# Optimization experiments

Measured on AMD Instinct MI355X. Metric: run time of the kernel, lower is better.

The kernel has to match this reference:

```python
import jax, jax.numpy as jnp
import numpy as np

D_IN = 1024
D_OUT = 1024


def setup_inputs() -> dict:
    key = jax.random.key(0)
    kx, kq, kk, kv = jax.random.split(key, 4)
    s = 1.0 / np.sqrt(D_IN)
    x = jax.random.normal(kx, (2, 4096, D_IN), dtype=jnp.float32)
    # nn.Linear weights: shape [d_out, d_in], y = x @ W.T (no bias)
    W_query = jax.random.normal(kq, (D_OUT, D_IN), dtype=jnp.float32) * s
    W_key = jax.random.normal(kk, (D_OUT, D_IN), dtype=jnp.float32) * s
    W_value = jax.random.normal(kv, (D_OUT, D_IN), dtype=jnp.float32) * s
    return {"x": x, "W_query": W_query, "W_key": W_key, "W_value": W_value}


def reference(x, W_query, W_key, W_value):
    # QKV projections: [b, n, d_in] @ [d_in, d_out]
    q = jnp.einsum('bnd,od->bno', x, W_query)
    k = jnp.einsum('bnd,od->bno', x, W_key)
    v = jnp.einsum('bnd,od->bno', x, W_value)
    d_k = k.shape[-1]
    scores = jnp.einsum('bqo,bko->bqk', q, k) / jnp.sqrt(jnp.asarray(d_k, x.dtype))
    # NOTE: source applies no causal mask despite the class name
    attn = jax.nn.softmax(scores, axis=-1)
    return jnp.einsum('bqk,bko->bqo', attn, v)
```

## Files before the change

### kernel.cpp

```cpp
#include <hip/hip_runtime.h>
#include <hip/hip_bf16.h>
#include <hip/hip_fp16.h>
#include <stdint.h>

typedef __bf16 bf16_t;
typedef __bf16 bf16x8 __attribute__((ext_vector_type(8)));
typedef float f32x4 __attribute__((ext_vector_type(4)));

typedef __attribute__((address_space(1))) void gv_t;
typedef __attribute__((address_space(3))) void lv_t;

__device__ inline unsigned short f2bf_bits(float f) {
  uint32_t u = __float_as_uint(f);
  u += 0x7FFFu + ((u >> 16) & 1u);
  return (unsigned short)(u >> 16);
}
__device__ inline bf16_t f2bf(float f) {
  unsigned short h = f2bf_bits(f);
  return __builtin_bit_cast(bf16_t, h);
}

__device__ inline void storeC(float* p, float v) { *p = v; }
__device__ inline void storeC(bf16_t* p, float v) { *p = f2bf(v); }
__device__ inline void storeC(__half* p, float v) { *p = __float2half(v); }

__global__ __launch_bounds__(256)
void convert_all(const float* __restrict__ x, const float* __restrict__ wq,
                 const float* __restrict__ wk, const float* __restrict__ wv,
                 bf16_t* __restrict__ xb, bf16_t* __restrict__ wqkb,
                 bf16_t* __restrict__ wvb)
{
  const int64_t NX = 8192LL * 1024, NW = 1024LL * 1024;
  const int64_t total4 = (NX + 3 * NW) >> 2;
  for (int64_t i = (int64_t)blockIdx.x * blockDim.x + threadIdx.x; i < total4;
       i += (int64_t)gridDim.x * blockDim.x) {
    int64_t e = i << 2;
    const float* src; bf16_t* dst; int64_t off;
    if (e < NX)               { src = x;  dst = xb;         off = e; }
    else if (e < NX + NW)     { src = wq; dst = wqkb;       off = e - NX; }
    else if (e < NX + 2 * NW) { src = wk; dst = wqkb + NW;  off = e - NX - NW; }
    else                      { src = wv; dst = wvb;        off = e - NX - 2 * NW; }
    float4 f = *(const float4*)(src + off);
    uint32_t lo = ((uint32_t)f2bf_bits(f.y) << 16) | f2bf_bits(f.x);
    uint32_t hi = ((uint32_t)f2bf_bits(f.w) << 16) | f2bf_bits(f.z);
    *(uint2*)(dst + off) = make_uint2(lo, hi);
  }
}

template <typename OUT_T>
__global__ __launch_bounds__(256)
void gemm_bt(const bf16_t* __restrict__ A, const bf16_t* __restrict__ B,
             OUT_T* __restrict__ C, int K, int lda, int ldb, int ldc,
             int64_t b_batch_stride, int bm_per_batch)
{
  __shared__ bf16_t As[2][128 * 32];
  __shared__ bf16_t Bs[2][128 * 32];
  const int tid  = threadIdx.x;
  const int wid  = tid >> 6;
  const int lane = tid & 63;
  const int wm = wid >> 1, wn = wid & 1;
  const int64_t bm = blockIdx.x;
  const int64_t bn = blockIdx.y;

  const bf16_t* Bb = B + (bm / bm_per_batch) * b_batch_stride;

  const int c0row = (wid * 2 + 0) * 16 + (lane >> 2);
  const int c1row = (wid * 2 + 1) * 16 + (lane >> 2);
  const int scol  = (lane & 3) * 8;

  const bf16_t* Ar0 = A  + (bm * 128 + c0row) * lda + scol;
  const bf16_t* Ar1 = A  + (bm * 128 + c1row) * lda + scol;
  const bf16_t* Br0 = Bb + (bn * 128 + c0row) * ldb + scol;
  const bf16_t* Br1 = Bb + (bn * 128 + c1row) * ldb + scol;

  const int ad0 = (wid * 2 + 0) * 512;
  const int ad1 = (wid * 2 + 1) * 512;

  const int frow = lane & 15;
  const int fk   = (lane >> 4) * 8;
  const int aoff = (wm * 64 + frow) * 32 + fk;
  const int boff = (wn * 64 + frow) * 32 + fk;

  f32x4 acc[4][4];
  #pragma unroll
  for (int m = 0; m < 4; m++)
    #pragma unroll
    for (int n = 0; n < 4; n++) acc[m][n] = f32x4{0.f, 0.f, 0.f, 0.f};

  auto stage = [&](int buf, int k0) {
    __builtin_amdgcn_global_load_lds((const gv_t*)(Ar0 + k0),
                                     (lv_t*)(&As[buf][ad0]), 16, 0, 0);
    __builtin_amdgcn_global_load_lds((const gv_t*)(Ar1 + k0),
                                     (lv_t*)(&As[buf][ad1]), 16, 0, 0);
    __builtin_amdgcn_global_load_lds((const gv_t*)(Br0 + k0),
                                     (lv_t*)(&Bs[buf][ad0]), 16, 0, 0);
    __builtin_amdgcn_global_load_lds((const gv_t*)(Br1 + k0),
                                     (lv_t*)(&Bs[buf][ad1]), 16, 0, 0);
  };

  stage(0, 0);
  __syncthreads();
  int cur = 0;
  for (int k0 = 0; k0 < K; k0 += 32) {
    if (k0 + 32 < K) stage(cur ^ 1, k0 + 32);

    bf16x8 af[4], bfr[4];
    #pragma unroll
    for (int m = 0; m < 4; m++)
      af[m] = *(const bf16x8*)(&As[cur][aoff + m * 16 * 32]);
    #pragma unroll
    for (int n = 0; n < 4; n++)
      bfr[n] = *(const bf16x8*)(&Bs[cur][boff + n * 16 * 32]);
    #pragma unroll
    for (int m = 0; m < 4; m++)
      #pragma unroll
      for (int n = 0; n < 4; n++)
        acc[m][n] = __builtin_amdgcn_mfma_f32_16x16x32_bf16(af[m], bfr[n],
                                                            acc[m][n], 0, 0, 0);
    __syncthreads();
    cur ^= 1;
  }

  const int crow = (lane >> 4) * 4;
  const int ccol = lane & 15;
  #pragma unroll
  for (int m = 0; m < 4; m++)
    #pragma unroll
    for (int n = 0; n < 4; n++)
      #pragma unroll
      for (int j = 0; j < 4; j++) {
        int64_t row = bm * 128 + wm * 64 + m * 16 + crow + j;
        int64_t col = bn * 128 + wn * 64 + n * 16 + ccol;
        storeC(&C[row * ldc + col], acc[m][n][j]);
      }
}

template <typename OUT_T, typename OUT2_T>
__global__ __launch_bounds__(512, 2)
void gemm256(const bf16_t* __restrict__ A, const bf16_t* __restrict__ B,
             OUT_T* __restrict__ C0, OUT2_T* __restrict__ C1,
             int K, int lda, int ldb, int ldc,
             int64_t b_batch_stride, int bm_per_batch,
             int64_t za_off, int64_t zb_off)
{
  __shared__ bf16_t As[2][256][64];
  __shared__ bf16_t Bs[2][256][64];

  const int tid  = threadIdx.x;
  const int wid  = tid >> 6;
  const int lane = tid & 63;
  const int wm = wid >> 2;
  const int wn = wid & 3;
  const int64_t bm = blockIdx.x;
  const int64_t bn = blockIdx.y;
  const int z = blockIdx.z;

  const bf16_t* Ap = A + (int64_t)z * za_off;
  const bf16_t* Bp = B + (bm / bm_per_batch) * b_batch_stride
                       + (int64_t)z * zb_off;

  const int srow  = wid * 16 + (lane >> 3);
  const int sslot = (lane & 7) ^ (lane >> 3);
  const int64_t lda64 = lda, ldb64 = ldb;
  const bf16_t* Ag = Ap + (bm * 256 + srow) * lda64 + sslot * 8;
  const bf16_t* Bg = Bp + (bn * 256 + srow) * ldb64 + sslot * 8;

  auto stageA = [&](int buf, int t, int h) {
    const bf16_t* src = Ag + (int64_t)(h * 128) * lda64 + t * 64;
    char* dst = (char*)&As[buf][h * 128 + wid * 16][0];
    __builtin_amdgcn_global_load_lds((const gv_t*)src, (lv_t*)dst, 16, 0, 0);
    __builtin_amdgcn_global_load_lds((const gv_t*)(src + 8 * lda64),
                                     (lv_t*)(dst + 1024), 16, 0, 0);
  };
  auto stageB = [&](int buf, int t, int h) {
    const bf16_t* src = Bg + (int64_t)(h * 128) * ldb64 + t * 64;
    char* dst = (char*)&Bs[buf][h * 128 + wid * 16][0];
    __builtin_amdgcn_global_load_lds((const gv_t*)src, (lv_t*)dst, 16, 0, 0);
    __builtin_amdgcn_global_load_lds((const gv_t*)(src + 8 * ldb64),
                                     (lv_t*)(dst + 1024), 16, 0, 0);
  };

  const int frow   = lane & 15;
  const int fcol16 = lane >> 4;
  const int xorv   = (lane & 7) << 4;
  const int ck0 = (fcol16 * 16) ^ xorv;
  const int ck1 = (64 + fcol16 * 16) ^ xorv;
  const int arowb = (wm * 128 + frow) * 128;
  const int browb = (wn * 64  + frow) * 128;

  f32x4 acc[8][4];
  #pragma unroll
  for (int m = 0; m < 8; m++)
    #pragma unroll
    for (int n = 0; n < 4; n++) acc[m][n] = f32x4{0.f, 0.f, 0.f, 0.f};

  const int NT = K >> 6;

  stageA(0, 0, 0); stageA(0, 0, 1);
  stageB(0, 0, 0); stageB(0, 0, 1);
  asm volatile("s_waitcnt vmcnt(0)" ::: "memory");
  __builtin_amdgcn_s_barrier();
  __builtin_amdgcn_sched_barrier(0);

  bf16x8 a[8][2], bb[4][2];

  for (int g = 0; g < NT; ++g) {
    const int buf = g & 1;
    const char* lA = (const char*)&As[buf][0][0];
    const char* lB = (const char*)&Bs[buf][0][0];

    #pragma unroll
    for (int m = 0; m < 8; m++)
      a[m][0] = *(const bf16x8*)(lA + arowb + m * 2048 + ck0);
    #pragma unroll
    for (int n = 0; n < 4; n++)
      bb[n][0] = *(const bf16x8*)(lB + browb + n * 2048 + ck0);
    #pragma unroll
    for (int m = 0; m < 8; m++)
      a[m][1] = *(const bf16x8*)(lA + arowb + m * 2048 + ck1);
    #pragma unroll
    for (int n = 0; n < 4; n++)
      bb[n][1] = *(const bf16x8*)(lB + browb + n * 2048 + ck1);

    if (g + 1 < NT) {
      stageA(buf ^ 1, g + 1, 0); stageA(buf ^ 1, g + 1, 1);
      stageB(buf ^ 1, g + 1, 0); stageB(buf ^ 1, g + 1, 1);
    }

    __builtin_amdgcn_s_setprio(1);
    #pragma unroll
    for (int k = 0; k < 2; k++)
      #pragma unroll
      for (int m = 0; m < 8; m++)
        #pragma unroll
        for (int n = 0; n < 4; n++)
          acc[m][n] = __builtin_amdgcn_mfma_f32_16x16x32_bf16(
              a[m][k], bb[n][k], acc[m][n], 0, 0, 0);
    __builtin_amdgcn_s_setprio(0);

    asm volatile("s_waitcnt vmcnt(0)" ::: "memory");
    __builtin_amdgcn_s_barrier();
    __builtin_amdgcn_sched_barrier(0);
  }

  const int crow = (lane >> 4) * 4;
  const int ccol = lane & 15;
  if (z == 0) {
    #pragma unroll
    for (int m = 0; m < 8; m++)
      #pragma unroll
      for (int n = 0; n < 4; n++)
        #pragma unroll
        for (int j = 0; j < 4; j++) {
          int64_t row = bm * 256 + wm * 128 + m * 16 + crow + j;
          int64_t col = bn * 256 + wn * 64 + n * 16 + ccol;
          storeC(&C0[row * (int64_t)ldc + col], acc[m][n][j]);
        }
  } else {
    #pragma unroll
    for (int m = 0; m < 8; m++)
      #pragma unroll
      for (int n = 0; n < 4; n++)
        #pragma unroll
        for (int j = 0; j < 4; j++) {
          int64_t row = bm * 256 + wm * 128 + m * 16 + crow + j;
          int64_t col = bn * 256 + wn * 64 + n * 16 + ccol;
          storeC(&C1[row * (int64_t)ldc + col], acc[m][n][j]);
        }
  }
}

__global__ __launch_bounds__(256)
void softmax_rows(__half* __restrict__ SP)
{
  const int64_t row = blockIdx.x;
  __half* s = SP + row * 4096;
  bf16_t* p = (bf16_t*)s;
  const int tid = threadIdx.x;
  const float scale = 0.03125f;

  float v[16];
  float vmax = -3.4e38f;
  #pragma unroll
  for (int i = 0; i < 4; i++) {
    uint2 raw = *(const uint2*)(s + i * 1024 + tid * 4);
    __half2 h01 = __builtin_bit_cast(__half2, raw.x);
    __half2 h23 = __builtin_bit_cast(__half2, raw.y);
    float2 f01 = __half22float2(h01);
    float2 f23 = __half22float2(h23);
    v[i * 4 + 0] = f01.x * scale;
    v[i * 4 + 1] = f01.y * scale;
    v[i * 4 + 2] = f23.x * scale;
    v[i * 4 + 3] = f23.y * scale;
    vmax = fmaxf(vmax, fmaxf(fmaxf(v[i*4+0], v[i*4+1]),
                             fmaxf(v[i*4+2], v[i*4+3])));
  }
  #pragma unroll
  for (int o = 32; o > 0; o >>= 1) vmax = fmaxf(vmax, __shfl_xor(vmax, o));
  __shared__ float redm[4];
  __shared__ float reds[4];
  if ((tid & 63) == 0) redm[tid >> 6] = vmax;
  __syncthreads();
  vmax = fmaxf(fmaxf(redm[0], redm[1]), fmaxf(redm[2], redm[3]));

  float lsum = 0.f;
  #pragma unroll
  for (int i = 0; i < 16; i++) {
    v[i] = __expf(v[i] - vmax);
    lsum += v[i];
  }
  #pragma unroll
  for (int o = 32; o > 0; o >>= 1) lsum += __shfl_xor(lsum, o);
  if ((tid & 63) == 0) reds[tid >> 6] = lsum;
  __syncthreads();
  lsum = (reds[0] + reds[1]) + (reds[2] + reds[3]);
  const float inv = 1.0f / lsum;

  #pragma unroll
  for (int i = 0; i < 4; i++) {
    uint32_t lo = ((uint32_t)f2bf_bits(v[i*4+1] * inv) << 16) | f2bf_bits(v[i*4+0] * inv);
    uint32_t hi = ((uint32_t)f2bf_bits(v[i*4+3] * inv) << 16) | f2bf_bits(v[i*4+2] * inv);
    *(uint2*)(p + i * 1024 + tid * 4) = make_uint2(lo, hi);
  }
}

__global__ __launch_bounds__(256)
void addk_h4(float4* __restrict__ o, const uint2* __restrict__ a, int64_t n4)
{
  for (int64_t i = (int64_t)blockIdx.x * blockDim.x + threadIdx.x; i < n4;
       i += (int64_t)gridDim.x * blockDim.x) {
    float4 x = o[i];
    uint2 raw = a[i];
    __half2 h01 = __builtin_bit_cast(__half2, raw.x);
    __half2 h23 = __builtin_bit_cast(__half2, raw.y);
    float2 f01 = __half22float2(h01);
    float2 f23 = __half22float2(h23);
    x.x += f01.x; x.y += f01.y; x.z += f23.x; x.w += f23.y;
    o[i] = x;
  }
}

extern "C" void kernel_launch(void* const* d_in, const int* in_sizes, int n_in,
                              void* d_out, int out_size, void* d_ws, size_t ws_size,
                              hipStream_t stream) {
  const float* x  = (const float*)d_in[0];
  const float* wq = (const float*)d_in[1];
  const float* wk = (const float*)d_in[2];
  const float* wv = (const float*)d_in[3];
  float* out = (float*)d_out;

  char* ws = (char*)d_ws;
  bf16_t* xb   = (bf16_t*)ws;
  bf16_t* wqkb = (bf16_t*)(ws + (16LL << 20));
  bf16_t* wvb  = (bf16_t*)(ws + (20LL << 20));
  __half* S    = (__half*)ws;
  bf16_t* qk   = (bf16_t*)(ws + (64LL << 20));
  __half* pk16 = (__half*)(ws + (64LL << 20));
  bf16_t* vt   = (bf16_t*)(ws + (96LL << 20));

  const int NO_BATCH = 1 << 30;

  convert_all<<<2048, 256, 0, stream>>>(x, wq, wk, wv, xb, wqkb, wvb);

  gemm256<bf16_t, bf16_t><<<dim3(32, 8, 1), 512, 0, stream>>>(
      xb, wqkb, qk, qk, 1024, 1024, 1024, 2048, 0, NO_BATCH, 0, 0);

  gemm_bt<bf16_t><<<dim3(8, 64), 256, 0, stream>>>(
      wvb, xb, vt, 1024, 1024, 1024, 8192, 0, NO_BATCH);

  gemm256<__half, __half><<<dim3(32, 16, 1), 512, 0, stream>>>(
      qk, qk + 1024, S, S, 1024, 2048, 2048, 4096, 4096LL * 2048, 16, 0, 0);

  softmax_rows<<<8192, 256, 0, stream>>>(S);

  gemm256<float, __half><<<dim3(32, 4, 2), 512, 0, stream>>>(
      (const bf16_t*)S, vt, out, pk16, 2048, 4096, 8192, 1024,
      4096, 16, 2048, 2048);

  addk_h4<<<2048, 256, 0, stream>>>((float4*)out, (const uint2*)pk16,
                                    8192LL * 1024 / 4);
}
```

Baseline: 230.6 us.

## Shrink GEMM tiles to 128x128 and reuse swizzled kernel for V projection

Replaces the 256x256-tile, 512-thread GEMM with a 128x128-tile, 256-thread variant that keeps the same XOR-swizzled LDS layout and double-buffered direct-to-LDS loads. The simple 32-wide-K gemm_bt used for the V-transpose projection is removed, and that projection now runs through the same kernel. Grids are rescaled, giving four times as many blocks per GEMM, which is meant to fill the CUs better and lower register and LDS pressure per block. In exchange each block does less data reuse per loaded byte, so global and L2 traffic rises.

```diff
diff --git a/kernel.cpp b/kernel.cpp
--- a/kernel.cpp
+++ b/kernel.cpp
@@ -47,110 +47,22 @@
   }
 }
 
-template <typename OUT_T>
-__global__ __launch_bounds__(256)
-void gemm_bt(const bf16_t* __restrict__ A, const bf16_t* __restrict__ B,
-             OUT_T* __restrict__ C, int K, int lda, int ldb, int ldc,
-             int64_t b_batch_stride, int bm_per_batch)
-{
-  __shared__ bf16_t As[2][128 * 32];
-  __shared__ bf16_t Bs[2][128 * 32];
-  const int tid  = threadIdx.x;
-  const int wid  = tid >> 6;
-  const int lane = tid & 63;
-  const int wm = wid >> 1, wn = wid & 1;
-  const int64_t bm = blockIdx.x;
-  const int64_t bn = blockIdx.y;
-
-  const bf16_t* Bb = B + (bm / bm_per_batch) * b_batch_stride;
-
-  const int c0row = (wid * 2 + 0) * 16 + (lane >> 2);
-  const int c1row = (wid * 2 + 1) * 16 + (lane >> 2);
-  const int scol  = (lane & 3) * 8;
-
-  const bf16_t* Ar0 = A  + (bm * 128 + c0row) * lda + scol;
-  const bf16_t* Ar1 = A  + (bm * 128 + c1row) * lda + scol;
-  const bf16_t* Br0 = Bb + (bn * 128 + c0row) * ldb + scol;
-  const bf16_t* Br1 = Bb + (bn * 128 + c1row) * ldb + scol;
-
-  const int ad0 = (wid * 2 + 0) * 512;
-  const int ad1 = (wid * 2 + 1) * 512;
-
-  const int frow = lane & 15;
-  const int fk   = (lane >> 4) * 8;
-  const int aoff = (wm * 64 + frow) * 32 + fk;
-  const int boff = (wn * 64 + frow) * 32 + fk;
-
-  f32x4 acc[4][4];
-  #pragma unroll
-  for (int m = 0; m < 4; m++)
-    #pragma unroll
-    for (int n = 0; n < 4; n++) acc[m][n] = f32x4{0.f, 0.f, 0.f, 0.f};
-
-  auto stage = [&](int buf, int k0) {
-    __builtin_amdgcn_global_load_lds((const gv_t*)(Ar0 + k0),
-                                     (lv_t*)(&As[buf][ad0]), 16, 0, 0);
-    __builtin_amdgcn_global_load_lds((const gv_t*)(Ar1 + k0),
-                                     (lv_t*)(&As[buf][ad1]), 16, 0, 0);
-    __builtin_amdgcn_global_load_lds((const gv_t*)(Br0 + k0),
-                                     (lv_t*)(&Bs[buf][ad0]), 16, 0, 0);
-    __builtin_amdgcn_global_load_lds((const gv_t*)(Br1 + k0),
-                                     (lv_t*)(&Bs[buf][ad1]), 16, 0, 0);
-  };
-
-  stage(0, 0);
-  __syncthreads();
-  int cur = 0;
-  for (int k0 = 0; k0 < K; k0 += 32) {
-    if (k0 + 32 < K) stage(cur ^ 1, k0 + 32);
-
-    bf16x8 af[4], bfr[4];
-    #pragma unroll
-    for (int m = 0; m < 4; m++)
-      af[m] = *(const bf16x8*)(&As[cur][aoff + m * 16 * 32]);
-    #pragma unroll
-    for (int n = 0; n < 4; n++)
-      bfr[n] = *(const bf16x8*)(&Bs[cur][boff + n * 16 * 32]);
-    #pragma unroll
-    for (int m = 0; m < 4; m++)
-      #pragma unroll
-      for (int n = 0; n < 4; n++)
-        acc[m][n] = __builtin_amdgcn_mfma_f32_16x16x32_bf16(af[m], bfr[n],
-                                                            acc[m][n], 0, 0, 0);
-    __syncthreads();
-    cur ^= 1;
-  }
-
-  const int crow = (lane >> 4) * 4;
-  const int ccol = lane & 15;
-  #pragma unroll
-  for (int m = 0; m < 4; m++)
-    #pragma unroll
-    for (int n = 0; n < 4; n++)
-      #pragma unroll
-      for (int j = 0; j < 4; j++) {
-        int64_t row = bm * 128 + wm * 64 + m * 16 + crow + j;
-        int64_t col = bn * 128 + wn * 64 + n * 16 + ccol;
-        storeC(&C[row * ldc + col], acc[m][n][j]);
-      }
-}
-
 template <typename OUT_T, typename OUT2_T>
-__global__ __launch_bounds__(512, 2)
-void gemm256(const bf16_t* __restrict__ A, const bf16_t* __restrict__ B,
+__global__ __launch_bounds__(256, 2)
+void gemm128(const bf16_t* __restrict__ A, const bf16_t* __restrict__ B,
              OUT_T* __restrict__ C0, OUT2_T* __restrict__ C1,
              int K, int lda, int ldb, int ldc,
              int64_t b_batch_stride, int bm_per_batch,
              int64_t za_off, int64_t zb_off)
 {
-  __shared__ bf16_t As[2][256][64];
-  __shared__ bf16_t Bs[2][256][64];
+  __shared__ bf16_t As[2][128][64];
+  __shared__ bf16_t Bs[2][128][64];
 
   const int tid  = threadIdx.x;
   const int wid  = tid >> 6;
   const int lane = tid & 63;
-  const int wm = wid >> 2;
-  const int wn = wid & 3;
+  const int wm = wid >> 1;
+  const int wn = wid & 1;
   const int64_t bm = blockIdx.x;
   const int64_t bn = blockIdx.y;
   const int z = blockIdx.z;
@@ -159,25 +71,21 @@
   const bf16_t* Bp = B + (bm / bm_per_batch) * b_batch_stride
                        + (int64_t)z * zb_off;
 
-  const int srow  = wid * 16 + (lane >> 3);
-  const int sslot = (lane & 7) ^ (lane >> 3);
+  const int srow  = tid >> 3;
+  const int sslot = (tid & 7) ^ (srow & 7);
   const int64_t lda64 = lda, ldb64 = ldb;
-  const bf16_t* Ag = Ap + (bm * 256 + srow) * lda64 + sslot * 8;
-  const bf16_t* Bg = Bp + (bn * 256 + srow) * ldb64 + sslot * 8;
-
-  auto stageA = [&](int buf, int t, int h) {
-    const bf16_t* src = Ag + (int64_t)(h * 128) * lda64 + t * 64;
-    char* dst = (char*)&As[buf][h * 128 + wid * 16][0];
+  const bf16_t* Ag = Ap + (bm * 128 + srow) * lda64 + sslot * 8;
+  const bf16_t* Bg = Bp + (bn * 128 + srow) * ldb64 + sslot * 8;
+
+  auto stageA = [&](int buf, int t, int q) {
+    const bf16_t* src = Ag + (int64_t)(q * 32) * lda64 + t * 64;
+    char* dst = (char*)&As[buf][0][0] + (q * 32 + wid * 8) * 128;
     __builtin_amdgcn_global_load_lds((const gv_t*)src, (lv_t*)dst, 16, 0, 0);
-    __builtin_amdgcn_global_load_lds((const gv_t*)(src + 8 * lda64),
-                                     (lv_t*)(dst + 1024), 16, 0, 0);
   };
-  auto stageB = [&](int buf, int t, int h) {
-    const bf16_t* src = Bg + (int64_t)(h * 128) * ldb64 + t * 64;
-    char* dst = (char*)&Bs[buf][h * 128 + wid * 16][0];
+  auto stageB = [&](int buf, int t, int q) {
+    const bf16_t* src = Bg + (int64_t)(q * 32) * ldb64 + t * 64;
+    char* dst = (char*)&Bs[buf][0][0] + (q * 32 + wid * 8) * 128;
     __builtin_amdgcn_global_load_lds((const gv_t*)src, (lv_t*)dst, 16, 0, 0);
-    __builtin_amdgcn_global_load_lds((const gv_t*)(src + 8 * ldb64),
-                                     (lv_t*)(dst + 1024), 16, 0, 0);
   };
 
   const int frow   = lane & 15;
@@ -185,24 +93,24 @@
   const int xorv   = (lane & 7) << 4;
   const int ck0 = (fcol16 * 16) ^ xorv;
   const int ck1 = (64 + fcol16 * 16) ^ xorv;
-  const int arowb = (wm * 128 + frow) * 128;
-  const int browb = (wn * 64  + frow) * 128;
-
-  f32x4 acc[8][4];
-  #pragma unroll
-  for (int m = 0; m < 8; m++)
+  const int arowb = (wm * 64 + frow) * 128;
+  const int browb = (wn * 64 + frow) * 128;
+
+  f32x4 acc[4][4];
+  #pragma unroll
+  for (int m = 0; m < 4; m++)
     #pragma unroll
     for (int n = 0; n < 4; n++) acc[m][n] = f32x4{0.f, 0.f, 0.f, 0.f};
 
   const int NT = K >> 6;
 
-  stageA(0, 0, 0); stageA(0, 0, 1);
-  stageB(0, 0, 0); stageB(0, 0, 1);
+  stageA(0, 0, 0); stageA(0, 0, 1); stageA(0, 0, 2); stageA(0, 0, 3);
+  stageB(0, 0, 0); stageB(0, 0, 1); stageB(0, 0, 2); stageB(0, 0, 3);
   asm volatile("s_waitcnt vmcnt(0)" ::: "memory");
   __builtin_amdgcn_s_barrier();
   __builtin_amdgcn_sched_barrier(0);
 
-  bf16x8 a[8][2], bb[4][2];
+  bf16x8 a[4][2], bb[4][2];
 
   for (int g = 0; g < NT; ++g) {
     const int buf = g & 1;
@@ -210,13 +118,13 @@
     const char* lB = (const char*)&Bs[buf][0][0];
 
     #pragma unroll
-    for (int m = 0; m < 8; m++)
+    for (int m = 0; m < 4; m++)
       a[m][0] = *(const bf16x8*)(lA + arowb + m * 2048 + ck0);
     #pragma unroll
     for (int n = 0; n < 4; n++)
       bb[n][0] = *(const bf16x8*)(lB + browb + n * 2048 + ck0);
     #pragma unroll
-    for (int m = 0; m < 8; m++)
+    for (int m = 0; m < 4; m++)
       a[m][1] = *(const bf16x8*)(lA + arowb + m * 2048 + ck1);
     #pragma unroll
     for (int n = 0; n < 4; n++)
@@ -224,14 +132,16 @@
 
     if (g + 1 < NT) {
       stageA(buf ^ 1, g + 1, 0); stageA(buf ^ 1, g + 1, 1);
+      stageA(buf ^ 1, g + 1, 2); stageA(buf ^ 1, g + 1, 3);
       stageB(buf ^ 1, g + 1, 0); stageB(buf ^ 1, g + 1, 1);
+      stageB(buf ^ 1, g + 1, 2); stageB(buf ^ 1, g + 1, 3);
     }
 
     __builtin_amdgcn_s_setprio(1);
     #pragma unroll
     for (int k = 0; k < 2; k++)
       #pragma unroll
-      for (int m = 0; m < 8; m++)
+      for (int m = 0; m < 4; m++)
         #pragma unroll
         for (int n = 0; n < 4; n++)
           acc[m][n] = __builtin_amdgcn_mfma_f32_16x16x32_bf16(
@@ -247,24 +157,24 @@
   const int ccol = lane & 15;
   if (z == 0) {
     #pragma unroll
-    for (int m = 0; m < 8; m++)
+    for (int m = 0; m < 4; m++)
       #pragma unroll
       for (int n = 0; n < 4; n++)
         #pragma unroll
         for (int j = 0; j < 4; j++) {
-          int64_t row = bm * 256 + wm * 128 + m * 16 + crow + j;
-          int64_t col = bn * 256 + wn * 64 + n * 16 + ccol;
+          int64_t row = bm * 128 + wm * 64 + m * 16 + crow + j;
+          int64_t col = bn * 128 + wn * 64 + n * 16 + ccol;
           storeC(&C0[row * (int64_t)ldc + col], acc[m][n][j]);
         }
   } else {
     #pragma unroll
-    for (int m = 0; m < 8; m++)
+    for (int m = 0; m < 4; m++)
       #pragma unroll
       for (int n = 0; n < 4; n++)
         #pragma unroll
         for (int j = 0; j < 4; j++) {
-          int64_t row = bm * 256 + wm * 128 + m * 16 + crow + j;
-          int64_t col = bn * 256 + wn * 64 + n * 16 + ccol;
+          int64_t row = bm * 128 + wm * 64 + m * 16 + crow + j;
+          int64_t col = bn * 128 + wn * 64 + n * 16 + ccol;
           storeC(&C1[row * (int64_t)ldc + col], acc[m][n][j]);
         }
   }
@@ -362,20 +272,20 @@
 
   convert_all<<<2048, 256, 0, stream>>>(x, wq, wk, wv, xb, wqkb, wvb);
 
-  gemm256<bf16_t, bf16_t><<<dim3(32, 8, 1), 512, 0, stream>>>(
+  gemm128<bf16_t, bf16_t><<<dim3(64, 16, 1), 256, 0, stream>>>(
       xb, wqkb, qk, qk, 1024, 1024, 1024, 2048, 0, NO_BATCH, 0, 0);
 
-  gemm_bt<bf16_t><<<dim3(8, 64), 256, 0, stream>>>(
-      wvb, xb, vt, 1024, 1024, 1024, 8192, 0, NO_BATCH);
-
-  gemm256<__half, __half><<<dim3(32, 16, 1), 512, 0, stream>>>(
-      qk, qk + 1024, S, S, 1024, 2048, 2048, 4096, 4096LL * 2048, 16, 0, 0);
+  gemm128<bf16_t, bf16_t><<<dim3(8, 64, 1), 256, 0, stream>>>(
+      wvb, xb, vt, vt, 1024, 1024, 1024, 8192, 0, NO_BATCH, 0, 0);
+
+  gemm128<__half, __half><<<dim3(64, 32, 1), 256, 0, stream>>>(
+      qk, qk + 1024, S, S, 1024, 2048, 2048, 4096, 4096LL * 2048, 32, 0, 0);
 
   softmax_rows<<<8192, 256, 0, stream>>>(S);
 
-  gemm256<float, __half><<<dim3(32, 4, 2), 512, 0, stream>>>(
+  gemm128<float, __half><<<dim3(64, 8, 2), 256, 0, stream>>>(
       (const bf16_t*)S, vt, out, pk16, 2048, 4096, 8192, 1024,
-      4096, 16, 2048, 2048);
+      4096, 32, 2048, 2048);
 
   addk_h4<<<2048, 256, 0, stream>>>((float4*)out, (const uint2*)pk16,
                                     8192LL * 1024 / 4);
```

Result: slower. 247.7 us (+7.4%).
